# Optimization experiments

Hardware: AMD Instinct MI355X
Metric: run time of the kernel (lower is better)

Reference implementation:

```python
import jax, jax.numpy as jnp
import numpy as np

HIDDEN = 2048
NUM_EXPERTS = 64
TOP_K = 2
LOAD_BALANCE_ALPHA = 0.01
Z_LOSS_ALPHA = 1e-4
TEMPERATURE = 1.0  # buffer init, clamped to [0.1, 2.0] -> 1.0


def setup_inputs() -> dict:
    key = jax.random.key(0)
    k1, k2 = jax.random.split(key)
    x = jax.random.normal(k1, (4, 4096, HIDDEN), dtype=jnp.float32)
    W = jax.random.normal(k2, (NUM_EXPERTS, HIDDEN), dtype=jnp.float32) * (1.0 / np.sqrt(HIDDEN))
    return {"x": x, "W": W}


def reference(x, W):
    # Eval-mode forward of RuchbahMoEGate.
    B, S, H = x.shape
    x_flat = x.reshape(-1, H)                       # [N, H], N = B*S
    logits = jnp.einsum('nh,eh->ne', x_flat, W)     # gate projection, [N, E]
    logits = logits / TEMPERATURE                   # temp clamped to [0.1,2.0]
    scores = jax.nn.softmax(logits, axis=-1)        # [N, E]
    # top-k routing (eval: dynamic top-k == top_k, no capacity limitation)
    top_scores, top_idx = jax.lax.top_k(scores, TOP_K)   # [N, K]
    top_scores = jax.nn.softmax(top_scores.astype(jnp.float32), axis=-1).astype(x.dtype)
    # load-balance loss (eval: total_routing_count == 0 -> basic term only)
    expert_load = scores.mean(axis=0)               # [E]
    ideal_load = 1.0 / NUM_EXPERTS
    lb_loss = LOAD_BALANCE_ALPHA * jnp.sum((expert_load - ideal_load) ** 2)
    # z-loss: penalize large logit logsumexp
    z_loss = Z_LOSS_ALPHA * jnp.mean(jax.nn.logsumexp(logits, axis=-1) ** 2)
    total_loss = lb_loss + z_loss
    return top_scores, top_idx, total_loss
```

## Files before the change

### kernel.cpp

```cpp
#include <hip/hip_runtime.h>
#include <cmath>
#include <cstdint>
#include <cstddef>

#define HDIM  2048
#define HHALF 1024
#define HC    16
#define NCHUNK (HHALF / HC)
#define NEXP  64
#define BTOK  64
#define PL    68

__global__ __launch_bounds__(256) void moe_fused(const float* __restrict__ x,
                                                 const float* __restrict__ W,
                                                 float* __restrict__ outS,
                                                 float* __restrict__ outI,
                                                 float* __restrict__ esumP,
                                                 float* __restrict__ lse2P,
                                                 int N) {
  __shared__ __align__(16) float xt[2][2][HC][PL];
  __shared__ __align__(16) float wt[2][2][HC][PL];
  __shared__ __align__(16) float lg[BTOK][PL];
  __shared__ float invS[BTOK];
  __shared__ float lseL[BTOK];
  __shared__ float esL[4][NEXP];

  const int b    = blockIdx.x;
  const int tok0 = b * BTOK;
  const int tid  = threadIdx.x;
  const int lane = tid & 63;
  const int w    = tid >> 6;
  const int eh   = w & 1;
  const int hh   = w >> 1;
  const int tg   = lane >> 3;
  const int eg   = lane & 7;
  const int row  = tid >> 2;
  const int cq   = tid & 3;

  const float* xp = x + (size_t)(tok0 + row) * HDIM + cq * 4;
  const float* wp = W + (size_t)row * HDIM + cq * 4;

  float acc[8][4];
#pragma unroll
  for (int t = 0; t < 8; ++t)
#pragma unroll
    for (int e = 0; e < 4; ++e) acc[t][e] = 0.f;

  {
    const float4 x0 = *reinterpret_cast<const float4*>(xp);
    const float4 x1 = *reinterpret_cast<const float4*>(xp + HHALF);
    const float4 w0 = *reinterpret_cast<const float4*>(wp);
    const float4 w1 = *reinterpret_cast<const float4*>(wp + HHALF);
    const int cc = cq * 4;
    xt[0][0][cc+0][row] = x0.x; xt[0][0][cc+1][row] = x0.y;
    xt[0][0][cc+2][row] = x0.z; xt[0][0][cc+3][row] = x0.w;
    xt[0][1][cc+0][row] = x1.x; xt[0][1][cc+1][row] = x1.y;
    xt[0][1][cc+2][row] = x1.z; xt[0][1][cc+3][row] = x1.w;
    wt[0][0][cc+0][row] = w0.x; wt[0][0][cc+1][row] = w0.y;
    wt[0][0][cc+2][row] = w0.z; wt[0][0][cc+3][row] = w0.w;
    wt[0][1][cc+0][row] = w1.x; wt[0][1][cc+1][row] = w1.y;
    wt[0][1][cc+2][row] = w1.z; wt[0][1][cc+3][row] = w1.w;
  }
  __syncthreads();

  const int trow = tg * 8;
  const int ecol = (eh << 5) + (eg << 2);

  int cur = 0;
  for (int c = 0; c < NCHUNK; ++c) {
    float4 x0, x1, w0, w1;
    const bool more = (c + 1 < NCHUNK);
    if (more) {
      const int off = (c + 1) * HC;
      x0 = *reinterpret_cast<const float4*>(xp + off);
      x1 = *reinterpret_cast<const float4*>(xp + HHALF + off);
      w0 = *reinterpret_cast<const float4*>(wp + off);
      w1 = *reinterpret_cast<const float4*>(wp + HHALF + off);
    }
#pragma unroll
    for (int h = 0; h < HC; ++h) {
      const float4 a0 = *reinterpret_cast<const float4*>(&xt[cur][hh][h][trow]);
      const float4 a1 = *reinterpret_cast<const float4*>(&xt[cur][hh][h][trow + 4]);
      const float4 bv = *reinterpret_cast<const float4*>(&wt[cur][hh][h][ecol]);
      const float xs[8] = {a0.x, a0.y, a0.z, a0.w, a1.x, a1.y, a1.z, a1.w};
      const float wv[4] = {bv.x, bv.y, bv.z, bv.w};
#pragma unroll
      for (int t = 0; t < 8; ++t)
#pragma unroll
        for (int e = 0; e < 4; ++e)
          acc[t][e] = fmaf(xs[t], wv[e], acc[t][e]);
    }
    if (more) {
      const int nb = cur ^ 1, cc = cq * 4;
      xt[nb][0][cc+0][row] = x0.x; xt[nb][0][cc+1][row] = x0.y;
      xt[nb][0][cc+2][row] = x0.z; xt[nb][0][cc+3][row] = x0.w;
      xt[nb][1][cc+0][row] = x1.x; xt[nb][1][cc+1][row] = x1.y;
      xt[nb][1][cc+2][row] = x1.z; xt[nb][1][cc+3][row] = x1.w;
      wt[nb][0][cc+0][row] = w0.x; wt[nb][0][cc+1][row] = w0.y;
      wt[nb][0][cc+2][row] = w0.z; wt[nb][0][cc+3][row] = w0.w;
      wt[nb][1][cc+0][row] = w1.x; wt[nb][1][cc+1][row] = w1.y;
      wt[nb][1][cc+2][row] = w1.z; wt[nb][1][cc+3][row] = w1.w;
    }
    __syncthreads();
    cur ^= 1;
  }

  if (hh == 0) {
#pragma unroll
    for (int t = 0; t < 8; ++t)
      *reinterpret_cast<float4*>(&lg[trow + t][ecol]) =
          make_float4(acc[t][0], acc[t][1], acc[t][2], acc[t][3]);
  }
  __syncthreads();
  if (hh == 1) {
#pragma unroll
    for (int t = 0; t < 8; ++t) {
      float4 cv = *reinterpret_cast<const float4*>(&lg[trow + t][ecol]);
      cv.x += acc[t][0]; cv.y += acc[t][1]; cv.z += acc[t][2]; cv.w += acc[t][3];
      *reinterpret_cast<float4*>(&lg[trow + t][ecol]) = cv;
    }
  }
  __syncthreads();

  if (lane < 16) {
    const int t = w * 16 + lane;
    float m = -INFINITY, v2 = -INFINITY;
    int i1 = 0, i2 = 0;
#pragma unroll
    for (int e4 = 0; e4 < 16; ++e4) {
      const float4 lv = *reinterpret_cast<const float4*>(&lg[t][e4 * 4]);
      const float ls[4] = {lv.x, lv.y, lv.z, lv.w};
#pragma unroll
      for (int j = 0; j < 4; ++j) {
        const float l = ls[j];
        const int e = e4 * 4 + j;
        if (l > m)       { v2 = m; i2 = i1; m = l; i1 = e; }
        else if (l > v2) { v2 = l; i2 = e; }
      }
    }
    float s = 0.f;
#pragma unroll
    for (int e4 = 0; e4 < 16; ++e4) {
      float4 lv = *reinterpret_cast<const float4*>(&lg[t][e4 * 4]);
      lv.x = expf(lv.x - m); s += lv.x;
      lv.y = expf(lv.y - m); s += lv.y;
      lv.z = expf(lv.z - m); s += lv.z;
      lv.w = expf(lv.w - m); s += lv.w;
      *reinterpret_cast<float4*>(&lg[t][e4 * 4]) = lv;
    }
    const float v1s = 1.f / s;
    const float v2s = expf(v2 - m) / s;
    const float mx  = fmaxf(v1s, v2s);
    const float e1  = expf(v1s - mx), e2 = expf(v2s - mx);
    const float inv = 1.f / (e1 + e2);
    *reinterpret_cast<float2*>(&outS[2 * (size_t)(tok0 + t)]) = make_float2(e1 * inv, e2 * inv);
    *reinterpret_cast<float2*>(&outI[2 * (size_t)(tok0 + t)]) = make_float2((float)i1, (float)i2);
    invS[t] = v1s;
    const float lse = m + logf(s);
    lseL[t] = lse * lse;
  }
  __syncthreads();

  float ea = 0.f;
#pragma unroll
  for (int i = 0; i < 16; ++i) {
    const int t = w * 16 + i;
    ea = fmaf(lg[t][lane], invS[t], ea);
  }
  esL[w][lane] = ea;
  __syncthreads();
  if (w == 0) {
    const float tot = ((esL[0][lane] + esL[1][lane]) + esL[2][lane]) + esL[3][lane];
    esumP[(size_t)b * NEXP + lane] = tot;
  }
  if (w == 1) {
    float la = lseL[lane];
#pragma unroll
    for (int d = 1; d < 64; d <<= 1) la += __shfl_xor(la, d);
    if (lane == 0) lse2P[b] = la;
  }
}

__global__ __launch_bounds__(256) void moe_loss(const float* __restrict__ esumP,
                                                const float* __restrict__ lse2P,
                                                float* __restrict__ outL,
                                                int N, int NB) {
  __shared__ float es4[4][NEXP];
  __shared__ float l4[4];
  const int tid = threadIdx.x, lane = tid & 63, w = tid >> 6;

  const int seg = NB / 4;
  float a = 0.f;
  for (int i = 0; i < seg; ++i)
    a += esumP[(size_t)(w * seg + i) * NEXP + lane];
  es4[w][lane] = a;

  float la = 0.f;
  for (int i = tid; i < NB; i += 256) la += lse2P[i];
#pragma unroll
  for (int d = 1; d < 64; d <<= 1) la += __shfl_xor(la, d);
  if (lane == 0) l4[w] = la;
  __syncthreads();

  if (tid < NEXP) {
    const float tot  = ((es4[0][tid] + es4[1][tid]) + es4[2][tid]) + es4[3][tid];
    const float load = tot / (float)N;
    const float dv   = load - 1.0f / 64.0f;
    float q = dv * dv;
#pragma unroll
    for (int d = 1; d < 64; d <<= 1) q += __shfl_xor(q, d);
    if (tid == 0) {
      const float lseSum = ((l4[0] + l4[1]) + l4[2]) + l4[3];
      outL[0] = 0.01f * q + 1e-4f * (lseSum / (float)N);
    }
  }
}

extern "C" void kernel_launch(void* const* d_in, const int* in_sizes, int n_in,
                              void* d_out, int out_size, void* d_ws, size_t ws_size,
                              hipStream_t stream) {
  const float* x = (const float*)d_in[0];
  const float* W = (const float*)d_in[1];
  const int N  = in_sizes[0] / HDIM;
  const int NB = N / BTOK;

  float* out  = (float*)d_out;
  float* outS = out;
  float* outI = out + (size_t)2 * N;
  float* outL = out + (size_t)4 * N;

  float* esumP = (float*)d_ws;
  float* lse2P = esumP + (size_t)NB * NEXP;

  moe_fused<<<dim3(NB), dim3(256), 0, stream>>>(x, W, outS, outI, esumP, lse2P, N);
  moe_loss<<<dim3(1), dim3(256), 0, stream>>>(esumP, lse2P, outL, N, NB);
}
```

Measured before the change: 256.0 us.

## Pre-transpose gate weights and restructure GEMM to per-token threads with swizzled LDS

Adds a small kernel that transposes W into an H-major layout in the workspace. The fused kernel then uses 512 threads, where each thread owns one token and 8 experts. It reads weights straight from global/L2 as wave-uniform vectors instead of staging them through LDS, and stores x tiles with an XOR swizzle to avoid bank conflicts. This drops the split-H reduction and halves LDS traffic for weights. The cost is an extra launch, plus possible register-level weight reuse loss and hardcoded N=16384 (NBLK=256) in the loss kernel.

```diff
diff --git a/kernel.cpp b/kernel.cpp
--- a/kernel.cpp
+++ b/kernel.cpp
@@ -3,153 +3,128 @@
 #include <cstdint>
 #include <cstddef>
 
-#define HDIM  2048
-#define HHALF 1024
-#define HC    16
-#define NCHUNK (HHALF / HC)
-#define NEXP  64
-#define BTOK  64
-#define PL    68
-
-__global__ __launch_bounds__(256) void moe_fused(const float* __restrict__ x,
-                                                 const float* __restrict__ W,
+#define HDIM 2048
+#define NEXP 64
+#define HC   64
+#define NCH  (HDIM / HC)
+#define BTOK 64
+#define NBLK 256
+#define LGP  68
+
+__global__ __launch_bounds__(256) void moe_wt(const float* __restrict__ W,
+                                              float* __restrict__ Wt) {
+  const int g = blockIdx.x * 256 + threadIdx.x;
+  Wt[g] = W[(g & 63) * HDIM + (g >> 6)];
+}
+
+__global__ __launch_bounds__(512) void moe_fused(const float* __restrict__ x,
+                                                 const float* __restrict__ Wt,
                                                  float* __restrict__ outS,
                                                  float* __restrict__ outI,
                                                  float* __restrict__ esumP,
-                                                 float* __restrict__ lse2P,
-                                                 int N) {
-  __shared__ __align__(16) float xt[2][2][HC][PL];
-  __shared__ __align__(16) float wt[2][2][HC][PL];
-  __shared__ __align__(16) float lg[BTOK][PL];
+                                                 float* __restrict__ lse2P) {
+  __shared__ __align__(16) float xt[2][BTOK][HC];
+  __shared__ __align__(16) float lg[BTOK][LGP];
   __shared__ float invS[BTOK];
   __shared__ float lseL[BTOK];
-  __shared__ float esL[4][NEXP];
+  __shared__ float esL[8][NEXP];
 
   const int b    = blockIdx.x;
   const int tok0 = b * BTOK;
   const int tid  = threadIdx.x;
-  const int lane = tid & 63;
-  const int w    = tid >> 6;
-  const int eh   = w & 1;
-  const int hh   = w >> 1;
-  const int tg   = lane >> 3;
-  const int eg   = lane & 7;
-  const int row  = tid >> 2;
-  const int cq   = tid & 3;
-
-  const float* xp = x + (size_t)(tok0 + row) * HDIM + cq * 4;
-  const float* wp = W + (size_t)row * HDIM + cq * 4;
-
-  float acc[8][4];
-#pragma unroll
-  for (int t = 0; t < 8; ++t)
-#pragma unroll
-    for (int e = 0; e < 4; ++e) acc[t][e] = 0.f;
+  const int t    = tid & 63;
+  const int wu   = __builtin_amdgcn_readfirstlane(tid >> 6);
+  const int e0   = wu << 3;
+
+  const int st  = tid >> 3;
+  const int sq  = tid & 7;
+  const float* xg = x + (size_t)(tok0 + st) * HDIM + (sq << 2);
+  char* xtb = (char*)&xt[0][0][0];
+  const int wb0 = st * 256 + ((sq ^ (st & 15)) << 4);
+  const int wb1 = st * 256 + (((sq + 8) ^ (st & 15)) << 4);
+
+  float acc[8];
+#pragma unroll
+  for (int e = 0; e < 8; ++e) acc[e] = 0.f;
 
   {
-    const float4 x0 = *reinterpret_cast<const float4*>(xp);
-    const float4 x1 = *reinterpret_cast<const float4*>(xp + HHALF);
-    const float4 w0 = *reinterpret_cast<const float4*>(wp);
-    const float4 w1 = *reinterpret_cast<const float4*>(wp + HHALF);
-    const int cc = cq * 4;
-    xt[0][0][cc+0][row] = x0.x; xt[0][0][cc+1][row] = x0.y;
-    xt[0][0][cc+2][row] = x0.z; xt[0][0][cc+3][row] = x0.w;
-    xt[0][1][cc+0][row] = x1.x; xt[0][1][cc+1][row] = x1.y;
-    xt[0][1][cc+2][row] = x1.z; xt[0][1][cc+3][row] = x1.w;
-    wt[0][0][cc+0][row] = w0.x; wt[0][0][cc+1][row] = w0.y;
-    wt[0][0][cc+2][row] = w0.z; wt[0][0][cc+3][row] = w0.w;
-    wt[0][1][cc+0][row] = w1.x; wt[0][1][cc+1][row] = w1.y;
-    wt[0][1][cc+2][row] = w1.z; wt[0][1][cc+3][row] = w1.w;
-  }
-  __syncthreads();
-
-  const int trow = tg * 8;
-  const int ecol = (eh << 5) + (eg << 2);
-
+    const float4 v0 = *reinterpret_cast<const float4*>(xg);
+    const float4 v1 = *reinterpret_cast<const float4*>(xg + 32);
+    *reinterpret_cast<float4*>(xtb + wb0) = v0;
+    *reinterpret_cast<float4*>(xtb + wb1) = v1;
+  }
+  __syncthreads();
+
+  const int sw = (t & 15) << 4;
   int cur = 0;
-  for (int c = 0; c < NCHUNK; ++c) {
-    float4 x0, x1, w0, w1;
-    const bool more = (c + 1 < NCHUNK);
+  for (int c = 0; c < NCH; ++c) {
+    float4 p0, p1;
+    const bool more = (c + 1 < NCH);
     if (more) {
-      const int off = (c + 1) * HC;
-      x0 = *reinterpret_cast<const float4*>(xp + off);
-      x1 = *reinterpret_cast<const float4*>(xp + HHALF + off);
-      w0 = *reinterpret_cast<const float4*>(wp + off);
-      w1 = *reinterpret_cast<const float4*>(wp + HHALF + off);
-    }
-#pragma unroll
-    for (int h = 0; h < HC; ++h) {
-      const float4 a0 = *reinterpret_cast<const float4*>(&xt[cur][hh][h][trow]);
-      const float4 a1 = *reinterpret_cast<const float4*>(&xt[cur][hh][h][trow + 4]);
-      const float4 bv = *reinterpret_cast<const float4*>(&wt[cur][hh][h][ecol]);
-      const float xs[8] = {a0.x, a0.y, a0.z, a0.w, a1.x, a1.y, a1.z, a1.w};
-      const float wv[4] = {bv.x, bv.y, bv.z, bv.w};
-#pragma unroll
-      for (int t = 0; t < 8; ++t)
-#pragma unroll
-        for (int e = 0; e < 4; ++e)
-          acc[t][e] = fmaf(xs[t], wv[e], acc[t][e]);
+      p0 = *reinterpret_cast<const float4*>(xg + (c + 1) * HC);
+      p1 = *reinterpret_cast<const float4*>(xg + (c + 1) * HC + 32);
+    }
+    const char*  rb   = xtb + cur * (BTOK * HC * 4) + t * 256;
+    const float* wrow = Wt + (c * HC) * NEXP + e0;
+#pragma unroll
+    for (int k = 0; k < 16; ++k) {
+      const float4 xv = *reinterpret_cast<const float4*>(rb + ((k << 4) ^ sw));
+      const float xs[4] = {xv.x, xv.y, xv.z, xv.w};
+      const float* wp = wrow + (k << 2) * NEXP;
+#pragma unroll
+      for (int j = 0; j < 4; ++j) {
+        const float4 wa = *reinterpret_cast<const float4*>(wp + j * NEXP);
+        const float4 wb = *reinterpret_cast<const float4*>(wp + j * NEXP + 4);
+        acc[0] = fmaf(xs[j], wa.x, acc[0]);
+        acc[1] = fmaf(xs[j], wa.y, acc[1]);
+        acc[2] = fmaf(xs[j], wa.z, acc[2]);
+        acc[3] = fmaf(xs[j], wa.w, acc[3]);
+        acc[4] = fmaf(xs[j], wb.x, acc[4]);
+        acc[5] = fmaf(xs[j], wb.y, acc[5]);
+        acc[6] = fmaf(xs[j], wb.z, acc[6]);
+        acc[7] = fmaf(xs[j], wb.w, acc[7]);
+      }
     }
     if (more) {
-      const int nb = cur ^ 1, cc = cq * 4;
-      xt[nb][0][cc+0][row] = x0.x; xt[nb][0][cc+1][row] = x0.y;
-      xt[nb][0][cc+2][row] = x0.z; xt[nb][0][cc+3][row] = x0.w;
-      xt[nb][1][cc+0][row] = x1.x; xt[nb][1][cc+1][row] = x1.y;
-      xt[nb][1][cc+2][row] = x1.z; xt[nb][1][cc+3][row] = x1.w;
-      wt[nb][0][cc+0][row] = w0.x; wt[nb][0][cc+1][row] = w0.y;
-      wt[nb][0][cc+2][row] = w0.z; wt[nb][0][cc+3][row] = w0.w;
-      wt[nb][1][cc+0][row] = w1.x; wt[nb][1][cc+1][row] = w1.y;
-      wt[nb][1][cc+2][row] = w1.z; wt[nb][1][cc+3][row] = w1.w;
+      char* nb = xtb + (cur ^ 1) * (BTOK * HC * 4);
+      *reinterpret_cast<float4*>(nb + wb0) = p0;
+      *reinterpret_cast<float4*>(nb + wb1) = p1;
     }
     __syncthreads();
     cur ^= 1;
   }
 
-  if (hh == 0) {
-#pragma unroll
-    for (int t = 0; t < 8; ++t)
-      *reinterpret_cast<float4*>(&lg[trow + t][ecol]) =
-          make_float4(acc[t][0], acc[t][1], acc[t][2], acc[t][3]);
-  }
-  __syncthreads();
-  if (hh == 1) {
-#pragma unroll
-    for (int t = 0; t < 8; ++t) {
-      float4 cv = *reinterpret_cast<const float4*>(&lg[trow + t][ecol]);
-      cv.x += acc[t][0]; cv.y += acc[t][1]; cv.z += acc[t][2]; cv.w += acc[t][3];
-      *reinterpret_cast<float4*>(&lg[trow + t][ecol]) = cv;
-    }
-  }
-  __syncthreads();
-
-  if (lane < 16) {
-    const int t = w * 16 + lane;
-    float m = -INFINITY, v2 = -INFINITY;
+  *reinterpret_cast<float4*>(&lg[t][e0])     = make_float4(acc[0], acc[1], acc[2], acc[3]);
+  *reinterpret_cast<float4*>(&lg[t][e0 + 4]) = make_float4(acc[4], acc[5], acc[6], acc[7]);
+  __syncthreads();
+
+  if (wu == 0) {
+    float m = -INFINITY, l2v = -INFINITY;
     int i1 = 0, i2 = 0;
 #pragma unroll
-    for (int e4 = 0; e4 < 16; ++e4) {
-      const float4 lv = *reinterpret_cast<const float4*>(&lg[t][e4 * 4]);
+    for (int k = 0; k < 16; ++k) {
+      const float4 lv = *reinterpret_cast<const float4*>(&lg[t][k << 2]);
       const float ls[4] = {lv.x, lv.y, lv.z, lv.w};
 #pragma unroll
       for (int j = 0; j < 4; ++j) {
         const float l = ls[j];
-        const int e = e4 * 4 + j;
-        if (l > m)       { v2 = m; i2 = i1; m = l; i1 = e; }
-        else if (l > v2) { v2 = l; i2 = e; }
+        const int e = (k << 2) + j;
+        if (l > m)        { l2v = m; i2 = i1; m = l; i1 = e; }
+        else if (l > l2v) { l2v = l; i2 = e; }
       }
     }
     float s = 0.f;
 #pragma unroll
-    for (int e4 = 0; e4 < 16; ++e4) {
-      float4 lv = *reinterpret_cast<const float4*>(&lg[t][e4 * 4]);
+    for (int k = 0; k < 16; ++k) {
+      float4 lv = *reinterpret_cast<const float4*>(&lg[t][k << 2]);
       lv.x = expf(lv.x - m); s += lv.x;
       lv.y = expf(lv.y - m); s += lv.y;
       lv.z = expf(lv.z - m); s += lv.z;
       lv.w = expf(lv.w - m); s += lv.w;
-      *reinterpret_cast<float4*>(&lg[t][e4 * 4]) = lv;
+      *reinterpret_cast<float4*>(&lg[t][k << 2]) = lv;
     }
     const float v1s = 1.f / s;
-    const float v2s = expf(v2 - m) / s;
+    const float v2s = expf(l2v - m) / s;
     const float mx  = fmaxf(v1s, v2s);
     const float e1  = expf(v1s - mx), e2 = expf(v2s - mx);
     const float inv = 1.f / (e1 + e2);
@@ -161,57 +136,64 @@
   }
   __syncthreads();
 
-  float ea = 0.f;
-#pragma unroll
-  for (int i = 0; i < 16; ++i) {
-    const int t = w * 16 + i;
-    ea = fmaf(lg[t][lane], invS[t], ea);
-  }
-  esL[w][lane] = ea;
-  __syncthreads();
-  if (w == 0) {
-    const float tot = ((esL[0][lane] + esL[1][lane]) + esL[2][lane]) + esL[3][lane];
-    esumP[(size_t)b * NEXP + lane] = tot;
-  }
-  if (w == 1) {
-    float la = lseL[lane];
+  {
+    float ea = 0.f;
+#pragma unroll
+    for (int i = 0; i < 8; ++i) {
+      const int tt = (wu << 3) + i;
+      ea = fmaf(lg[tt][t], invS[tt], ea);
+    }
+    esL[wu][t] = ea;
+  }
+  __syncthreads();
+  if (wu == 0) {
+    float tot = esL[0][t];
+#pragma unroll
+    for (int w2 = 1; w2 < 8; ++w2) tot += esL[w2][t];
+    esumP[(size_t)t * NBLK + b] = tot;
+  }
+  if (wu == 1) {
+    float la = lseL[t];
 #pragma unroll
     for (int d = 1; d < 64; d <<= 1) la += __shfl_xor(la, d);
-    if (lane == 0) lse2P[b] = la;
+    if (t == 0) lse2P[b] = la;
   }
 }
 
 __global__ __launch_bounds__(256) void moe_loss(const float* __restrict__ esumP,
                                                 const float* __restrict__ lse2P,
-                                                float* __restrict__ outL,
-                                                int N, int NB) {
-  __shared__ float es4[4][NEXP];
+                                                float* __restrict__ outL, int N) {
+  __shared__ float esF[NEXP];
   __shared__ float l4[4];
   const int tid = threadIdx.x, lane = tid & 63, w = tid >> 6;
 
-  const int seg = NB / 4;
+  const int e = tid >> 2, q = tid & 3;
+  const float4* colp = reinterpret_cast<const float4*>(&esumP[(size_t)e * NBLK + q * 64]);
   float a = 0.f;
-  for (int i = 0; i < seg; ++i)
-    a += esumP[(size_t)(w * seg + i) * NEXP + lane];
-  es4[w][lane] = a;
-
-  float la = 0.f;
-  for (int i = tid; i < NB; i += 256) la += lse2P[i];
+#pragma unroll
+  for (int i = 0; i < 16; ++i) {
+    const float4 t4 = colp[i];
+    a += ((t4.x + t4.y) + t4.z) + t4.w;
+  }
+  a += __shfl_xor(a, 1);
+  a += __shfl_xor(a, 2);
+  if (q == 0) esF[e] = a;
+
+  float la = lse2P[tid];
 #pragma unroll
   for (int d = 1; d < 64; d <<= 1) la += __shfl_xor(la, d);
   if (lane == 0) l4[w] = la;
   __syncthreads();
 
   if (tid < NEXP) {
-    const float tot  = ((es4[0][tid] + es4[1][tid]) + es4[2][tid]) + es4[3][tid];
-    const float load = tot / (float)N;
+    const float load = esF[tid] / (float)N;
     const float dv   = load - 1.0f / 64.0f;
-    float q = dv * dv;
-#pragma unroll
-    for (int d = 1; d < 64; d <<= 1) q += __shfl_xor(q, d);
+    float qq = dv * dv;
+#pragma unroll
+    for (int d = 1; d < 64; d <<= 1) qq += __shfl_xor(qq, d);
     if (tid == 0) {
       const float lseSum = ((l4[0] + l4[1]) + l4[2]) + l4[3];
-      outL[0] = 0.01f * q + 1e-4f * (lseSum / (float)N);
+      outL[0] = 0.01f * qq + 1e-4f * (lseSum / (float)N);
     }
   }
 }
@@ -221,17 +203,18 @@
                               hipStream_t stream) {
   const float* x = (const float*)d_in[0];
   const float* W = (const float*)d_in[1];
-  const int N  = in_sizes[0] / HDIM;
-  const int NB = N / BTOK;
+  const int N = in_sizes[0] / HDIM;
 
   float* out  = (float*)d_out;
   float* outS = out;
   float* outI = out + (size_t)2 * N;
   float* outL = out + (size_t)4 * N;
 
-  float* esumP = (float*)d_ws;
-  float* lse2P = esumP + (size_t)NB * NEXP;
-
-  moe_fused<<<dim3(NB), dim3(256), 0, stream>>>(x, W, outS, outI, esumP, lse2P, N);
-  moe_loss<<<dim3(1), dim3(256), 0, stream>>>(esumP, lse2P, outL, N, NB);
-}
+  float* Wt    = (float*)d_ws;
+  float* esumP = Wt + (size_t)HDIM * NEXP;
+  float* lse2P = esumP + (size_t)NEXP * NBLK;
+
+  moe_wt<<<dim3((HDIM * NEXP) / 256), dim3(256), 0, stream>>>(W, Wt);
+  moe_fused<<<dim3(N / BTOK), dim3(512), 0, stream>>>(x, Wt, outS, outI, esumP, lse2P);
+  moe_loss<<<dim3(1), dim3(256), 0, stream>>>(esumP, lse2P, outL, N);
+}
```

After: 636.5 us. +148.7%, slower.
